# Performance work log

Measured on AMD Instinct MI355X. Metric: run time of the kernel, lower is better.

The kernel has to match this reference:

```python
import jax, jax.numpy as jnp
import numpy as np

B, N, C, H, W = 4, 24, 256, 100, 100
SCALE = 0.25      # feature-map stride scale (MultiScaleRoIAlign spatial scale)
OUT = 7           # output_size
SR = 2            # sampling_ratio
IMG = H / SCALE   # image size in box coordinates (400)


def setup_inputs() -> dict:
    key = jax.random.key(0)
    kf, kx, ky, kw, kh = jax.random.split(key, 5)
    features = jax.random.normal(kf, (B, C, H, W), dtype=jnp.float32)
    # valid boxes: positive height/width (module asserts non-degenerate boxes)
    x1 = jax.random.uniform(kx, (B, N), minval=0.0, maxval=IMG * 0.6)
    y1 = jax.random.uniform(ky, (B, N), minval=0.0, maxval=IMG * 0.6)
    bw = jax.random.uniform(kw, (B, N), minval=16.0, maxval=IMG * 0.35)
    bh = jax.random.uniform(kh, (B, N), minval=16.0, maxval=IMG * 0.35)
    x2 = jnp.minimum(x1 + bw, IMG - 1.0)
    y2 = jnp.minimum(y1 + bh, IMG - 1.0)
    boxes = jnp.stack([x1, y1, x2, y2], axis=-1)  # [B, N, 4] xyxy
    return {"features": features, "boxes": boxes}


def _roi_align(features, rois, batch_ix):
    """torchvision-style RoIAlign (aligned=False). rois: [R,4] xyxy in image coords."""
    R = rois.shape[0]
    x1, y1, x2, y2 = [rois[:, i] * SCALE for i in range(4)]
    roi_w = jnp.maximum(x2 - x1, 1.0)
    roi_h = jnp.maximum(y2 - y1, 1.0)
    bin_w = roi_w / OUT
    bin_h = roi_h / OUT
    # sample-point offsets within the roi: (bin + (k+0.5)/SR) for k in [0,SR)
    grid = (jnp.arange(OUT, dtype=jnp.float32)[:, None]
            + (jnp.arange(SR, dtype=jnp.float32)[None, :] + 0.5) / SR).reshape(-1)  # [OUT*SR]
    ys = y1[:, None] + grid[None, :] * bin_h[:, None]  # [R, 14]
    xs = x1[:, None] + grid[None, :] * bin_w[:, None]  # [R, 14]
    Y = ys[:, :, None]  # [R,14,1]
    X = xs[:, None, :]  # [R,1,14]
    valid = (Y > -1.0) & (Y < H) & (X > -1.0) & (X < W)  # [R,14,14]
    Yc = jnp.clip(Y, 0.0, H - 1.0)
    Xc = jnp.clip(X, 0.0, W - 1.0)
    y0f = jnp.floor(Yc); x0f = jnp.floor(Xc)
    ly = Yc - y0f; lx = Xc - x0f
    hy = 1.0 - ly;  hx = 1.0 - lx
    y0 = y0f.astype(jnp.int32); x0 = x0f.astype(jnp.int32)
    y1i = jnp.minimum(y0 + 1, H - 1); x1i = jnp.minimum(x0 + 1, W - 1)
    b = batch_ix[:, None, None]
    # gathers -> [R,14,14,C] each (advanced indices around the ':' put C last)
    f00 = features[b, :, y0,  x0]
    f01 = features[b, :, y0,  x1i]
    f10 = features[b, :, y1i, x0]
    f11 = features[b, :, y1i, x1i]
    w00 = (hy * hx)[..., None]; w01 = (hy * lx)[..., None]
    w10 = (ly * hx)[..., None]; w11 = (ly * lx)[..., None]
    val = (w00 * f00 + w01 * f01 + w10 * f10 + w11 * f11) * valid[..., None]
    # average SRxSR samples per bin -> [R, OUT, OUT, C] -> [R, C, OUT, OUT]
    pooled = val.reshape(R, OUT, SR, OUT, SR, C).mean(axis=(2, 4))
    return pooled.transpose(0, 3, 1, 2)


def reference(features, boxes):
    # 1) pairwise union boxes (vectorized form of _single_image_expand)
    iu, ju = jnp.triu_indices(N, k=1)          # P pairs, i<j
    b1 = boxes[:, iu]                          # [B, P, 4]
    b2 = boxes[:, ju]
    union = jnp.concatenate([jnp.minimum(b1[..., :2], b2[..., :2]),
                             jnp.maximum(b1[..., 2:], b2[..., 2:])], axis=-1)
    rois = jnp.concatenate([boxes, union], axis=1)  # [B, M, 4], M = N + P
    M = rois.shape[1]
    batch_ix = jnp.repeat(jnp.arange(B), M)
    pooled = _roi_align(features, rois.reshape(-1, 4), batch_ix)  # [B*M, C, 7, 7]
    pooled = pooled.reshape(B, M, C, OUT, OUT)
    # 2) pair assembly (vectorized _ObjPairLayer): [obj_i, obj_j, union_ij]
    obj = pooled[:, :N]    # [B, N, C, 7, 7]
    uni = pooled[:, N:]    # [B, P, C, 7, 7]
    pair_feats = jnp.stack([obj[:, iu], obj[:, ju], uni], axis=2)  # [B, P, 3, C, 7, 7]
    P = iu.shape[0]
    return pair_feats.reshape(B * P, 3, C, OUT, OUT)
```

## Files before the change

### kernel.cpp

```cpp
#include <hip/hip_runtime.h>

#define B_    4
#define N_OBJ 24
#define C_    256
#define H_    100
#define W_    100
#define HW_   (H_ * W_)
#define OUT_  7
#define P_    276
#define M_    (N_OBJ + P_)
#define SCALE_ 0.25f
#define CHW_OUT (C_ * OUT_ * OUT_)

typedef float f4_t __attribute__((ext_vector_type(4)));

__device__ __forceinline__ void pair_from_p(int p, int& i, int& j) {
    int ii = 0, rem = p;
    while (rem >= N_OBJ - 1 - ii) { rem -= (N_OBJ - 1 - ii); ++ii; }
    i = ii; j = ii + 1 + rem;
}

__global__ __launch_bounds__(256) void transpose_kernel(
        const float* __restrict__ feat, float* __restrict__ featT) {
    __shared__ float tile[64][65];
    const int b   = blockIdx.z;
    const int c0  = blockIdx.y * 64;
    const int px0 = blockIdx.x * 64;
    const int t   = threadIdx.x;
    const int cl  = t >> 6;
    const int px  = t & 63;
#pragma unroll
    for (int k = 0; k < 16; ++k) {
        const int c_loc = cl + k * 4;
        const int gpx   = px0 + px;
        tile[c_loc][px] = (gpx < HW_)
            ? feat[((size_t)b * C_ + c0 + c_loc) * HW_ + gpx] : 0.0f;
    }
    __syncthreads();
    const int c2 = t & 63;
    const int pl = t >> 6;
#pragma unroll
    for (int k = 0; k < 16; ++k) {
        const int px_l = pl + k * 4;
        const int gpx  = px0 + px_l;
        if (gpx < HW_)
            featT[((size_t)b * HW_ + gpx) * C_ + c0 + c2] = tile[c2][px_l];
    }
}

__global__ __launch_bounds__(256) void roi_kernel(
        const float* __restrict__ featT,
        const float* __restrict__ boxes,
        float* __restrict__ out,
        float* __restrict__ ws_obj) {
    __shared__ float lds[CHW_OUT];
    const int xcd = blockIdx.x & 7;
    const int b   = xcd >> 1;
    const int m   = ((blockIdx.x >> 3) << 1) | (xcd & 1);

    float x1, y1, x2, y2;
    if (m < N_OBJ) {
        const float* bp = boxes + ((size_t)b * N_OBJ + m) * 4;
        x1 = bp[0]; y1 = bp[1]; x2 = bp[2]; y2 = bp[3];
    } else {
        int i, j; pair_from_p(m - N_OBJ, i, j);
        const float* b1 = boxes + ((size_t)b * N_OBJ + i) * 4;
        const float* b2 = boxes + ((size_t)b * N_OBJ + j) * 4;
        x1 = fminf(b1[0], b2[0]); y1 = fminf(b1[1], b2[1]);
        x2 = fmaxf(b1[2], b2[2]); y2 = fmaxf(b1[3], b2[3]);
    }
    x1 *= SCALE_; y1 *= SCALE_; x2 *= SCALE_; y2 *= SCALE_;
    const float bin_w = fmaxf(x2 - x1, 1.0f) * (1.0f / OUT_);
    const float bin_h = fmaxf(y2 - y1, 1.0f) * (1.0f / OUT_);

    const int lane = threadIdx.x & 63;
    const int wv   = threadIdx.x >> 6;
    const f4_t* fbase = (const f4_t*)(featT + (size_t)b * HW_ * C_) + lane;

    for (int s = wv; s < OUT_ * OUT_; s += 4) {
        const int ph = s / OUT_, pw = s - ph * OUT_;

        float ywt[2][2]; int yi[2][2];
#pragma unroll
        for (int iy = 0; iy < 2; ++iy) {
            const float Y  = y1 + ((float)ph + (iy ? 0.75f : 0.25f)) * bin_h;
            const float vy = (Y > -1.0f && Y < (float)H_) ? 1.0f : 0.0f;
            const float Yc = fminf(fmaxf(Y, 0.0f), (float)(H_ - 1));
            const int  y0  = (int)floorf(Yc);
            const float ly = Yc - (float)y0;
            yi[iy][0] = y0; yi[iy][1] = min(y0 + 1, H_ - 1);
            ywt[iy][0] = vy * (1.0f - ly); ywt[iy][1] = vy * ly;
        }
        float xwt[2][2]; int xi[2][2];
#pragma unroll
        for (int ix = 0; ix < 2; ++ix) {
            const float X  = x1 + ((float)pw + (ix ? 0.75f : 0.25f)) * bin_w;
            const float vx = (X > -1.0f && X < (float)W_) ? 0.25f : 0.0f;
            const float Xc = fminf(fmaxf(X, 0.0f), (float)(W_ - 1));
            const int  x0  = (int)floorf(Xc);
            const float lx = Xc - (float)x0;
            xi[ix][0] = x0; xi[ix][1] = min(x0 + 1, W_ - 1);
            xwt[ix][0] = vx * (1.0f - lx); xwt[ix][1] = vx * lx;
        }

        int   offs[16]; float wts[16];
#pragma unroll
        for (int k = 0; k < 16; ++k) {
            const int iy = k >> 3, ix = (k >> 2) & 1, cy = (k >> 1) & 1, cx = k & 1;
            offs[k] = (yi[iy][cy] * W_ + xi[ix][cx]) * (C_ / 4);
            wts[k]  = ywt[iy][cy] * xwt[ix][cx];
        }
        f4_t f[16];
#pragma unroll
        for (int k = 0; k < 16; ++k) f[k] = fbase[offs[k]];
        f4_t acc = (f4_t){0.f, 0.f, 0.f, 0.f};
#pragma unroll
        for (int k = 0; k < 16; ++k) acc += wts[k] * f[k];

        const int c0 = lane * 4;
        lds[(c0 + 0) * 49 + s] = acc.x;
        lds[(c0 + 1) * 49 + s] = acc.y;
        lds[(c0 + 2) * 49 + s] = acc.z;
        lds[(c0 + 3) * 49 + s] = acc.w;
    }
    __syncthreads();

    const f4_t* s4 = (const f4_t*)lds;
    if (m < N_OBJ) {
        f4_t* d4 = (f4_t*)(ws_obj + ((size_t)b * N_OBJ + m) * CHW_OUT);
        for (int idx = threadIdx.x; idx < CHW_OUT / 4; idx += 256)
            d4[idx] = s4[idx];
    } else {
        f4_t* d4 = (f4_t*)(out + (((size_t)(b * P_ + (m - N_OBJ))) * 3 + 2) * CHW_OUT);
        for (int idx = threadIdx.x; idx < CHW_OUT / 4; idx += 256)
            __builtin_nontemporal_store(s4[idx], d4 + idx);
    }
}

__global__ __launch_bounds__(256) void assemble_kernel(
        const float* __restrict__ ws_obj, float* __restrict__ out) {
    const int bp   = blockIdx.x;
    const int slot = blockIdx.y;
    const int b = bp / P_;
    const int p = bp - b * P_;
    int i, j; pair_from_p(p, i, j);
    const int n = slot ? j : i;
    const f4_t* src = (const f4_t*)(ws_obj + ((size_t)b * N_OBJ + n) * CHW_OUT);
    f4_t* dst = (f4_t*)(out + (((size_t)bp) * 3 + slot) * CHW_OUT);
    for (int idx = threadIdx.x; idx < CHW_OUT / 4; idx += 256)
        __builtin_nontemporal_store(src[idx], dst + idx);
}

extern "C" void kernel_launch(void* const* d_in, const int* in_sizes, int n_in,
                              void* d_out, int out_size, void* d_ws, size_t ws_size,
                              hipStream_t stream) {
    const float* feat  = (const float*)d_in[0];
    const float* boxes = (const float*)d_in[1];
    float* out = (float*)d_out;

    float* featT  = (float*)d_ws;
    float* ws_obj = featT + (size_t)B_ * HW_ * C_;

    transpose_kernel<<<dim3((HW_ + 63) / 64, C_ / 64, B_), 256, 0, stream>>>(feat, featT);
    roi_kernel<<<B_ * M_, 256, 0, stream>>>(featT, boxes, out, ws_obj);
    assemble_kernel<<<dim3(B_ * P_, 2), 256, 0, stream>>>(ws_obj, out);
}
```

Before: 252.6 us.

## Fuse pair assembly into ROI kernel and skip duplicate bilinear taps

Removes the separate assemble kernel and the object workspace: each per-object block now writes its pooled result directly into every pair slot it belongs to, with object blocks scheduled first. Bilinear sample rows/columns that map to the same pixel are merged and loads with zero weight are skipped. This saves a launch and the workspace write/read, but concentrates many output writes in 96 blocks, which may create a tail.

New measurement: 248.5 us. About the same (-1.6%).

```diff
diff --git a/kernel.cpp b/kernel.cpp
--- a/kernel.cpp
+++ b/kernel.cpp
@@ -13,12 +13,6 @@
 #define CHW_OUT (C_ * OUT_ * OUT_)
 
 typedef float f4_t __attribute__((ext_vector_type(4)));
-
-__device__ __forceinline__ void pair_from_p(int p, int& i, int& j) {
-    int ii = 0, rem = p;
-    while (rem >= N_OBJ - 1 - ii) { rem -= (N_OBJ - 1 - ii); ++ii; }
-    i = ii; j = ii + 1 + rem;
-}
 
 __global__ __launch_bounds__(256) void transpose_kernel(
         const float* __restrict__ feat, float* __restrict__ featT) {
@@ -48,24 +42,34 @@
     }
 }
 
-__global__ __launch_bounds__(256) void roi_kernel(
+__global__ __launch_bounds__(256) void roi_fused_kernel(
         const float* __restrict__ featT,
         const float* __restrict__ boxes,
-        float* __restrict__ out,
-        float* __restrict__ ws_obj) {
+        float* __restrict__ out) {
     __shared__ float lds[CHW_OUT];
-    const int xcd = blockIdx.x & 7;
-    const int b   = xcd >> 1;
-    const int m   = ((blockIdx.x >> 3) << 1) | (xcd & 1);
+    const int blk    = blockIdx.x;
+    const bool is_obj = blk < B_ * N_OBJ;
+    int b, m;
+    if (is_obj) {
+        b = (blk & 7) >> 1;
+        m = ((blk >> 3) << 1) | (blk & 1);
+    } else {
+        const int t = blk - B_ * N_OBJ;
+        b = (t & 7) >> 1;
+        m = N_OBJ + (((t >> 3) << 1) | (t & 1));
+    }
 
     float x1, y1, x2, y2;
-    if (m < N_OBJ) {
+    if (is_obj) {
         const float* bp = boxes + ((size_t)b * N_OBJ + m) * 4;
         x1 = bp[0]; y1 = bp[1]; x2 = bp[2]; y2 = bp[3];
     } else {
-        int i, j; pair_from_p(m - N_OBJ, i, j);
-        const float* b1 = boxes + ((size_t)b * N_OBJ + i) * 4;
-        const float* b2 = boxes + ((size_t)b * N_OBJ + j) * 4;
+        int p = m - N_OBJ;
+        int ii = 0, rem = p;
+        while (rem >= N_OBJ - 1 - ii) { rem -= (N_OBJ - 1 - ii); ++ii; }
+        const int jj = ii + 1 + rem;
+        const float* b1 = boxes + ((size_t)b * N_OBJ + ii) * 4;
+        const float* b2 = boxes + ((size_t)b * N_OBJ + jj) * 4;
         x1 = fminf(b1[0], b2[0]); y1 = fminf(b1[1], b2[1]);
         x2 = fmaxf(b1[2], b2[2]); y2 = fmaxf(b1[3], b2[3]);
     }
@@ -80,42 +84,71 @@
     for (int s = wv; s < OUT_ * OUT_; s += 4) {
         const int ph = s / OUT_, pw = s - ph * OUT_;
 
-        float ywt[2][2]; int yi[2][2];
-#pragma unroll
-        for (int iy = 0; iy < 2; ++iy) {
-            const float Y  = y1 + ((float)ph + (iy ? 0.75f : 0.25f)) * bin_h;
-            const float vy = (Y > -1.0f && Y < (float)H_) ? 1.0f : 0.0f;
-            const float Yc = fminf(fmaxf(Y, 0.0f), (float)(H_ - 1));
-            const int  y0  = (int)floorf(Yc);
-            const float ly = Yc - (float)y0;
-            yi[iy][0] = y0; yi[iy][1] = min(y0 + 1, H_ - 1);
-            ywt[iy][0] = vy * (1.0f - ly); ywt[iy][1] = vy * ly;
+        int ri_[4]; float rw_[4];
+        {
+            const float Ya = y1 + ((float)ph + 0.25f) * bin_h;
+            const float Yb = y1 + ((float)ph + 0.75f) * bin_h;
+            const float va = (Ya > -1.0f && Ya < (float)H_) ? 1.0f : 0.0f;
+            const float vb = (Yb > -1.0f && Yb < (float)H_) ? 1.0f : 0.0f;
+            const float Yca = fminf(fmaxf(Ya, 0.0f), (float)(H_ - 1));
+            const float Ycb = fminf(fmaxf(Yb, 0.0f), (float)(H_ - 1));
+            const int y0a = (int)floorf(Yca);
+            const int y0b = (int)floorf(Ycb);
+            const float lya = Yca - (float)y0a;
+            const float lyb = Ycb - (float)y0b;
+            ri_[0] = y0a; ri_[1] = min(y0a + 1, H_ - 1);
+            ri_[2] = y0b; ri_[3] = min(y0b + 1, H_ - 1);
+            rw_[0] = va * (1.0f - lya); rw_[1] = va * lya;
+            rw_[2] = vb * (1.0f - lyb); rw_[3] = vb * lyb;
+            if (ri_[1] == ri_[0]) { rw_[0] += rw_[1]; rw_[1] = 0.0f; }
+            if (ri_[3] == ri_[2]) { rw_[2] += rw_[3]; rw_[3] = 0.0f; }
+            if (ri_[2] == ri_[0]) {
+                rw_[0] += rw_[2]; rw_[1] += rw_[3]; rw_[2] = 0.0f; rw_[3] = 0.0f;
+            } else if (ri_[2] == ri_[1]) {
+                rw_[1] += rw_[2]; rw_[2] = 0.0f;
+            }
         }
-        float xwt[2][2]; int xi[2][2];
-#pragma unroll
-        for (int ix = 0; ix < 2; ++ix) {
-            const float X  = x1 + ((float)pw + (ix ? 0.75f : 0.25f)) * bin_w;
-            const float vx = (X > -1.0f && X < (float)W_) ? 0.25f : 0.0f;
-            const float Xc = fminf(fmaxf(X, 0.0f), (float)(W_ - 1));
-            const int  x0  = (int)floorf(Xc);
-            const float lx = Xc - (float)x0;
-            xi[ix][0] = x0; xi[ix][1] = min(x0 + 1, W_ - 1);
-            xwt[ix][0] = vx * (1.0f - lx); xwt[ix][1] = vx * lx;
+        int ci_[4]; float cw_[4];
+        {
+            const float Xa = x1 + ((float)pw + 0.25f) * bin_w;
+            const float Xb = x1 + ((float)pw + 0.75f) * bin_w;
+            const float va = (Xa > -1.0f && Xa < (float)W_) ? 0.25f : 0.0f;
+            const float vb = (Xb > -1.0f && Xb < (float)W_) ? 0.25f : 0.0f;
+            const float Xca = fminf(fmaxf(Xa, 0.0f), (float)(W_ - 1));
+            const float Xcb = fminf(fmaxf(Xb, 0.0f), (float)(W_ - 1));
+            const int x0a = (int)floorf(Xca);
+            const int x0b = (int)floorf(Xcb);
+            const float lxa = Xca - (float)x0a;
+            const float lxb = Xcb - (float)x0b;
+            ci_[0] = x0a; ci_[1] = min(x0a + 1, W_ - 1);
+            ci_[2] = x0b; ci_[3] = min(x0b + 1, W_ - 1);
+            cw_[0] = va * (1.0f - lxa); cw_[1] = va * lxa;
+            cw_[2] = vb * (1.0f - lxb); cw_[3] = vb * lxb;
+            if (ci_[1] == ci_[0]) { cw_[0] += cw_[1]; cw_[1] = 0.0f; }
+            if (ci_[3] == ci_[2]) { cw_[2] += cw_[3]; cw_[3] = 0.0f; }
+            if (ci_[2] == ci_[0]) {
+                cw_[0] += cw_[2]; cw_[1] += cw_[3]; cw_[2] = 0.0f; cw_[3] = 0.0f;
+            } else if (ci_[2] == ci_[1]) {
+                cw_[1] += cw_[2]; cw_[2] = 0.0f;
+            }
         }
 
         int   offs[16]; float wts[16];
 #pragma unroll
-        for (int k = 0; k < 16; ++k) {
-            const int iy = k >> 3, ix = (k >> 2) & 1, cy = (k >> 1) & 1, cx = k & 1;
-            offs[k] = (yi[iy][cy] * W_ + xi[ix][cx]) * (C_ / 4);
-            wts[k]  = ywt[iy][cy] * xwt[ix][cx];
-        }
+        for (int r = 0; r < 4; ++r)
+#pragma unroll
+            for (int c = 0; c < 4; ++c) {
+                offs[r * 4 + c] = (ri_[r] * W_ + ci_[c]) * (C_ / 4);
+                wts[r * 4 + c]  = rw_[r] * cw_[c];
+            }
         f4_t f[16];
 #pragma unroll
-        for (int k = 0; k < 16; ++k) f[k] = fbase[offs[k]];
+        for (int k = 0; k < 16; ++k)
+            if (wts[k] != 0.0f) f[k] = fbase[offs[k]];
         f4_t acc = (f4_t){0.f, 0.f, 0.f, 0.f};
 #pragma unroll
-        for (int k = 0; k < 16; ++k) acc += wts[k] * f[k];
+        for (int k = 0; k < 16; ++k)
+            if (wts[k] != 0.0f) acc += wts[k] * f[k];
 
         const int c0 = lane * 4;
         lds[(c0 + 0) * 49 + s] = acc.x;
@@ -126,29 +159,22 @@
     __syncthreads();
 
     const f4_t* s4 = (const f4_t*)lds;
-    if (m < N_OBJ) {
-        f4_t* d4 = (f4_t*)(ws_obj + ((size_t)b * N_OBJ + m) * CHW_OUT);
-        for (int idx = threadIdx.x; idx < CHW_OUT / 4; idx += 256)
-            d4[idx] = s4[idx];
-    } else {
-        f4_t* d4 = (f4_t*)(out + (((size_t)(b * P_ + (m - N_OBJ))) * 3 + 2) * CHW_OUT);
+    if (!is_obj) {
+        const int p = m - N_OBJ;
+        f4_t* d4 = (f4_t*)(out + (((size_t)(b * P_ + p)) * 3 + 2) * CHW_OUT);
         for (int idx = threadIdx.x; idx < CHW_OUT / 4; idx += 256)
             __builtin_nontemporal_store(s4[idx], d4 + idx);
+    } else {
+        for (int q = 0; q < N_OBJ; ++q) {
+            if (q == m) continue;
+            const int i = min(m, q), j = max(m, q);
+            const int p = i * (2 * N_OBJ - i - 1) / 2 + (j - i - 1);
+            const int slot = (m < q) ? 0 : 1;
+            f4_t* d4 = (f4_t*)(out + (((size_t)(b * P_ + p)) * 3 + slot) * CHW_OUT);
+            for (int idx = threadIdx.x; idx < CHW_OUT / 4; idx += 256)
+                __builtin_nontemporal_store(s4[idx], d4 + idx);
+        }
     }
-}
-
-__global__ __launch_bounds__(256) void assemble_kernel(
-        const float* __restrict__ ws_obj, float* __restrict__ out) {
-    const int bp   = blockIdx.x;
-    const int slot = blockIdx.y;
-    const int b = bp / P_;
-    const int p = bp - b * P_;
-    int i, j; pair_from_p(p, i, j);
-    const int n = slot ? j : i;
-    const f4_t* src = (const f4_t*)(ws_obj + ((size_t)b * N_OBJ + n) * CHW_OUT);
-    f4_t* dst = (f4_t*)(out + (((size_t)bp) * 3 + slot) * CHW_OUT);
-    for (int idx = threadIdx.x; idx < CHW_OUT / 4; idx += 256)
-        __builtin_nontemporal_store(src[idx], dst + idx);
 }
 
 extern "C" void kernel_launch(void* const* d_in, const int* in_sizes, int n_in,
@@ -158,10 +184,8 @@
     const float* boxes = (const float*)d_in[1];
     float* out = (float*)d_out;
 
-    float* featT  = (float*)d_ws;
-    float* ws_obj = featT + (size_t)B_ * HW_ * C_;
+    float* featT = (float*)d_ws;
 
     transpose_kernel<<<dim3((HW_ + 63) / 64, C_ / 64, B_), 256, 0, stream>>>(feat, featT);
-    roi_kernel<<<B_ * M_, 256, 0, stream>>>(featT, boxes, out, ws_obj);
-    assemble_kernel<<<dim3(B_ * P_, 2), 256, 0, stream>>>(ws_obj, out);
+    roi_fused_kernel<<<B_ * M_, 256, 0, stream>>>(featT, boxes, out);
 }
```
